# Performance work log

Hardware: AMD Instinct MI355X
Metric: run time of the kernel (lower is better)

## Reference

```python
import jax, jax.numpy as jnp
import numpy as np

N_NODES = 100000
N_EDGES = 1600000
D_IN = 128
D_OUT = 128
NEG_SLOPE = 0.01  # torch F.leaky_relu default


def setup_inputs() -> dict:
    key = jax.random.key(0)
    k1, k2, k3, k4, k5 = jax.random.split(key, 5)
    h = jax.random.normal(k1, (N_NODES, D_IN), dtype=jnp.float32)
    # nn.Linear default init scale ~ 1/sqrt(fan_in)
    W = jax.random.normal(k2, (D_IN, D_OUT), dtype=jnp.float32) / np.sqrt(D_IN)
    attn_w = jax.random.normal(k3, (2 * D_OUT,), dtype=jnp.float32) / np.sqrt(2 * D_OUT)
    edge_src = jax.random.randint(k4, (N_EDGES,), 0, N_NODES, dtype=jnp.int32)
    edge_dst = jax.random.randint(k5, (N_EDGES,), 0, N_NODES, dtype=jnp.int32)
    return {"h": h, "W": W, "attn_w": attn_w, "edge_src": edge_src, "edge_dst": edge_dst}


def reference(h, W, attn_w, edge_src, edge_dst):
    n = h.shape[0]
    d = W.shape[1]
    z = h @ W                                   # [N, d]
    # attention_func(cat([z_src, z_dst])) == z_src @ a[:d] + z_dst @ a[d:]
    s_src = z @ attn_w[:d]                      # [N]
    s_dst = z @ attn_w[d:]                      # [N]
    e = jax.nn.leaky_relu(s_src[edge_src] + s_dst[edge_dst], NEG_SLOPE)  # [E]
    # segment softmax over incoming edges of each dst node
    m = jax.ops.segment_max(e, edge_dst, num_segments=n)   # [N], -inf for empty
    ex = jnp.exp(e - m[edge_dst])                           # [E]
    denom = jax.ops.segment_sum(ex, edge_dst, num_segments=n)  # [N]
    alpha = ex / denom[edge_dst]                             # [E]
    # weighted neighbor sum: sum_j alpha_ij * z_j
    out = jax.ops.segment_sum(alpha[:, None] * z[edge_src], edge_dst, num_segments=n)
    return out
```

## Files before the change

### kernel.cpp

```cpp
#include <hip/hip_runtime.h>

#define D 128
#define NEG_SLOPE 0.01f
#define BSHIFT 7
#define B1 1024
#define SCHUNK 4096
#define SLOT 2560

typedef __attribute__((ext_vector_type(8))) short short8;
typedef __attribute__((ext_vector_type(4))) float floatx4;

__device__ __forceinline__ unsigned f2bf_rne(float x) {
    unsigned u = __float_as_uint(x);
    return (u + 0x7fffu + ((u >> 16) & 1u)) >> 16;
}
#define BF_LO(u) __uint_as_float((u) << 16)
#define BF_HI(u) __uint_as_float((u) & 0xffff0000u)

__global__ __launch_bounds__(256) void prep_wfrag(const float* __restrict__ W,
                                                  unsigned short* __restrict__ whi,
                                                  unsigned short* __restrict__ wlo,
                                                  int* __restrict__ gcur) {
    if (blockIdx.x == 0) {
        for (int i = threadIdx.x; i < B1; i += 256) gcur[i] = i * SLOT;
    }
    const int idx = blockIdx.x * 256 + threadIdx.x;
    const int j    = idx & 7;
    const int lane = (idx >> 3) & 63;
    const int tk   = idx >> 9;
    const int kk = tk & 3, ct = tk >> 2;
    const int k = kk * 32 + (lane >> 4) * 8 + j;
    const int n = ct * 16 + (lane & 15);
    const float x = W[k * D + n];
    const unsigned hi = f2bf_rne(x);
    const float hf = __uint_as_float(hi << 16);
    whi[idx] = (unsigned short)hi;
    wlo[idx] = (unsigned short)(__float_as_uint(x - hf) >> 16);
}

__global__ __launch_bounds__(1024) void sort_scatter(const int* __restrict__ esrc,
                                                     const int* __restrict__ edst,
                                                     int* __restrict__ gcur,
                                                     int* __restrict__ pairs, int E) {
    __shared__ int cnt[B1], exc[B1], gbs[B1], cur[B1];
    __shared__ int spk[SCHUNK];
    __shared__ unsigned short sbkt[SCHUNK];
    __shared__ int wtot[16];
    const int t = threadIdx.x;
    const int lane = t & 63, wv = t >> 6;
    cnt[t] = 0; cur[t] = 0;
    __syncthreads();

    const int e0 = blockIdx.x * SCHUNK;
    const int n  = min(SCHUNK, E - e0);

    int pk[4], bk[4];
    const int i0 = t * 4;
    if (i0 + 3 < n) {
        const int4 dv = *(const int4*)&edst[e0 + i0];
        const int4 sv = *(const int4*)&esrc[e0 + i0];
        const int dd[4] = {dv.x, dv.y, dv.z, dv.w};
        const int ss[4] = {sv.x, sv.y, sv.z, sv.w};
#pragma unroll
        for (int k = 0; k < 4; ++k) {
            bk[k] = dd[k] >> BSHIFT;
            pk[k] = (ss[k] << BSHIFT) | (dd[k] & 127);
            atomicAdd(&cnt[bk[k]], 1);
        }
    } else {
#pragma unroll
        for (int k = 0; k < 4; ++k) {
            const int i = i0 + k;
            if (i < n) {
                const int d = edst[e0 + i];
                const int s = esrc[e0 + i];
                bk[k] = d >> BSHIFT;
                pk[k] = (s << BSHIFT) | (d & 127);
                atomicAdd(&cnt[bk[k]], 1);
            } else {
                bk[k] = -1;
            }
        }
    }
    __syncthreads();

    const int c = cnt[t];
    int incl = c;
#pragma unroll
    for (int o = 1; o < 64; o <<= 1) {
        int v = __shfl_up(incl, o, 64);
        if (lane >= o) incl += v;
    }
    if (lane == 63) wtot[wv] = incl;
    __syncthreads();
    int wpre = 0;
#pragma unroll
    for (int i = 0; i < 16; ++i) wpre += (i < wv) ? wtot[i] : 0;
    exc[t] = wpre + incl - c;
    if (c > 0) gbs[t] = atomicAdd(&gcur[t], c);
    __syncthreads();

#pragma unroll
    for (int k = 0; k < 4; ++k) {
        if (bk[k] >= 0) {
            const int p = exc[bk[k]] + atomicAdd(&cur[bk[k]], 1);
            spk[p]  = pk[k];
            sbkt[p] = (unsigned short)bk[k];
        }
    }
    __syncthreads();

    for (int i = t; i < n; i += 1024) {
        const int b = sbkt[i];
        const int pos = gbs[b] + (i - exc[b]);
        if (pos < (b + 1) * SLOT) pairs[pos] = spk[i];
    }
}

__global__ __launch_bounds__(256) void fine_build(const int* __restrict__ pairs,
                                                  const int* __restrict__ gcur,
                                                  int* __restrict__ beg,
                                                  int* __restrict__ ncnt,
                                                  int* __restrict__ adj, int N) {
    __shared__ int cnt[128], sc[128], cur[128];
    const int b = blockIdx.x;
    const int base = b << BSHIFT;
    const int nd = min(128, N - base);
    const int t = threadIdx.x;
    const int s0 = b * SLOT;
    const int e1 = min(gcur[b], s0 + SLOT);
    if (t < 128) { cnt[t] = 0; cur[t] = 0; }
    __syncthreads();
    for (int i = s0 + t; i < e1; i += 256)
        atomicAdd(&cnt[pairs[i] & 127], 1);
    __syncthreads();
    if (t < 128) sc[t] = cnt[t];
    __syncthreads();
    for (int off = 1; off < 128; off <<= 1) {
        int v = (t < 128 && t >= off) ? sc[t - off] : 0;
        __syncthreads();
        if (t < 128) sc[t] += v;
        __syncthreads();
    }
    if (t < nd) {
        beg[base + t]  = s0 + sc[t] - cnt[t];
        ncnt[base + t] = cnt[t];
    }
    __syncthreads();
    for (int i = s0 + t; i < e1; i += 256) {
        const int pkv = pairs[i];
        const int d = pkv & 127;
        const int pos = s0 + (sc[d] - cnt[d]) + atomicAdd(&cur[d], 1);
        adj[pos] = pkv >> BSHIFT;
    }
}

__global__ __launch_bounds__(256) void gemm_zs(const float* __restrict__ h,
                                               const unsigned short* __restrict__ whi,
                                               const unsigned short* __restrict__ wlo,
                                               const float* __restrict__ aw,
                                               unsigned short* __restrict__ z,
                                               float* __restrict__ s_src,
                                               float* __restrict__ s_dst, int N) {
    const int t = threadIdx.x;
    const int lane = t & 63, quad = lane >> 4, l16 = lane & 15;
    const int rowbase = blockIdx.x * 64 + (t >> 6) * 16;
    const int arow = min(rowbase + l16, N - 1);
    const float* __restrict__ hrow = h + (size_t)arow * D;

    floatx4 acc[8];
#pragma unroll
    for (int ct = 0; ct < 8; ++ct) acc[ct] = (floatx4){0.f, 0.f, 0.f, 0.f};

#pragma unroll
    for (int kk = 0; kk < 4; ++kk) {
        const int k0 = kk * 32 + quad * 8;
        float4 x0 = *(const float4*)&hrow[k0];
        float4 x1 = *(const float4*)&hrow[k0 + 4];
        float xs[8] = {x0.x, x0.y, x0.z, x0.w, x1.x, x1.y, x1.z, x1.w};
        union { short8 v; unsigned short u[8]; } ahi, alo;
#pragma unroll
        for (int i = 0; i < 8; ++i) {
            unsigned hi = f2bf_rne(xs[i]);
            float hf = __uint_as_float(hi << 16);
            ahi.u[i] = (unsigned short)hi;
            alo.u[i] = (unsigned short)(__float_as_uint(xs[i] - hf) >> 16);
        }
#pragma unroll
        for (int ct = 0; ct < 8; ++ct) {
            const int fo = ((ct * 4 + kk) * 64 + lane) * 8;
            short8 bhi = *(const short8*)&whi[fo];
            short8 blo = *(const short8*)&wlo[fo];
            acc[ct] = __builtin_amdgcn_mfma_f32_16x16x32_bf16(ahi.v, bhi, acc[ct], 0, 0, 0);
            acc[ct] = __builtin_amdgcn_mfma_f32_16x16x32_bf16(alo.v, bhi, acc[ct], 0, 0, 0);
            acc[ct] = __builtin_amdgcn_mfma_f32_16x16x32_bf16(ahi.v, blo, acc[ct], 0, 0, 0);
        }
    }

#pragma unroll
    for (int ct = 0; ct < 8; ++ct)
#pragma unroll
        for (int reg = 0; reg < 4; ++reg) {
            int r = rowbase + quad * 4 + reg;
            if (r < N)
                z[(size_t)r * D + ct * 16 + l16] = (unsigned short)f2bf_rne(acc[ct][reg]);
        }

    float ps[4] = {0.f, 0.f, 0.f, 0.f}, pd[4] = {0.f, 0.f, 0.f, 0.f};
#pragma unroll
    for (int ct = 0; ct < 8; ++ct) {
        float as = aw[ct * 16 + l16];
        float ad = aw[128 + ct * 16 + l16];
#pragma unroll
        for (int reg = 0; reg < 4; ++reg) {
            ps[reg] = fmaf(acc[ct][reg], as, ps[reg]);
            pd[reg] = fmaf(acc[ct][reg], ad, pd[reg]);
        }
    }
#pragma unroll
    for (int reg = 0; reg < 4; ++reg)
#pragma unroll
        for (int o = 1; o < 16; o <<= 1) {
            ps[reg] += __shfl_xor(ps[reg], o, 64);
            pd[reg] += __shfl_xor(pd[reg], o, 64);
        }
    if (l16 == 0) {
#pragma unroll
        for (int reg = 0; reg < 4; ++reg) {
            int r = rowbase + quad * 4 + reg;
            if (r < N) { s_src[r] = ps[reg]; s_dst[r] = pd[reg]; }
        }
    }
}

__global__ __launch_bounds__(256) void aggregate(const unsigned short* __restrict__ z,
                                                 const float* __restrict__ s_src,
                                                 const float* __restrict__ s_dst,
                                                 const int* __restrict__ beg_,
                                                 const int* __restrict__ ncnt_,
                                                 const int* __restrict__ adj,
                                                 float* __restrict__ out,
                                                 int nodeBase, int nEnd) {
    const int lane = threadIdx.x & 63;
    const int half = lane >> 5;
    const int l32  = lane & 31;
    const int q2   = l32 >> 4;
    const int l16  = lane & 15;
    const int hb   = half << 5;
    const int pairBase = nodeBase + blockIdx.x * 8 + (threadIdx.x >> 6) * 2;
    if (pairBase >= nEnd) return;
    const int nodeA = pairBase, nodeB = pairBase + 1;
    const int cA = ncnt_[nodeA], bA = beg_[nodeA];
    int cB = 0, bB = 0;
    if (nodeB < nEnd) { cB = ncnt_[nodeB]; bB = beg_[nodeB]; }

    auto fma8 = [&](float* ac, float w, const uint4& v) {
        ac[0] = fmaf(w, BF_LO(v.x), ac[0]); ac[1] = fmaf(w, BF_HI(v.x), ac[1]);
        ac[2] = fmaf(w, BF_LO(v.y), ac[2]); ac[3] = fmaf(w, BF_HI(v.y), ac[3]);
        ac[4] = fmaf(w, BF_LO(v.z), ac[4]); ac[5] = fmaf(w, BF_HI(v.z), ac[5]);
        ac[6] = fmaf(w, BF_LO(v.w), ac[6]); ac[7] = fmaf(w, BF_HI(v.w), ac[7]);
    };

    if (max(cA, cB) <= 32) {
        const int myn = pairBase + half;
        const int valid = myn < nEnd;
        const int mb  = half ? bB : bA;
        const int mc  = half ? cB : cA;
        const float sd = s_dst[valid ? myn : 0];
        int s = 0; float e = -INFINITY;
        if (l32 < mc) {
            s = adj[mb + l32];
            float tt = s_src[s] + sd;
            e = (tt >= 0.f) ? tt : NEG_SLOPE * tt;
        }
        int sj[4]; uint4 zv[4];
#pragma unroll
        for (int u = 0; u < 4; ++u) sj[u] = __shfl(s, hb + u * 2 + q2, 64);
#pragma unroll
        for (int u = 0; u < 4; ++u)
            zv[u] = *(const uint4*)&z[(size_t)sj[u] * D + l16 * 8];

        float mx = e;
#pragma unroll
        for (int o = 16; o; o >>= 1) mx = fmaxf(mx, __shfl_xor(mx, o, 64));
        float ex = (l32 < mc) ? __expf(e - mx) : 0.f;
        float sum = ex;
#pragma unroll
        for (int o = 16; o; o >>= 1) sum += __shfl_xor(sum, o, 64);
        const float inv = (mc > 0) ? 1.f / sum : 0.f;
        const float w = ex * inv;

        float a[8] = {0.f,0.f,0.f,0.f,0.f,0.f,0.f,0.f};
        float bacc[8] = {0.f,0.f,0.f,0.f,0.f,0.f,0.f,0.f};
#pragma unroll
        for (int u = 0; u < 4; ++u) {
            const int ji = u * 2 + q2;
            float wj = __shfl(w, hb + ji, 64);
            wj = (ji < mc) ? wj : 0.f;
            fma8((u & 1) ? bacc : a, wj, zv[u]);
        }
        for (int jj = 8; jj < mc; jj += 8) {
            int ji2[4]; float wj[4]; int sj2[4];
#pragma unroll
            for (int u = 0; u < 4; ++u) {
                ji2[u] = jj + u * 2 + q2;
                wj[u]  = __shfl(w, hb + ji2[u], 64);
                sj2[u] = __shfl(s, hb + ji2[u], 64);
                wj[u]  = (ji2[u] < mc) ? wj[u] : 0.f;
            }
            uint4 z0 = *(const uint4*)&z[(size_t)sj2[0] * D + l16 * 8];
            uint4 z1 = *(const uint4*)&z[(size_t)sj2[1] * D + l16 * 8];
            uint4 z2 = *(const uint4*)&z[(size_t)sj2[2] * D + l16 * 8];
            uint4 z3 = *(const uint4*)&z[(size_t)sj2[3] * D + l16 * 8];
            fma8(a, wj[0], z0);
            fma8(bacc, wj[1], z1);
            fma8(a, wj[2], z2);
            fma8(bacc, wj[3], z3);
        }
#pragma unroll
        for (int i = 0; i < 8; ++i) {
            a[i] += bacc[i];
            a[i] += __shfl_xor(a[i], 16, 64);
        }
        if (q2 == 0 && valid) {
            float* o = &out[(size_t)myn * D + l16 * 8];
            *(float4*)o       = make_float4(a[0], a[1], a[2], a[3]);
            *(float4*)(o + 4) = make_float4(a[4], a[5], a[6], a[7]);
        }
        return;
    }

    const int q = lane >> 4;
    for (int which = 0; which < 2; ++which) {
        const int myn = which ? nodeB : nodeA;
        if (myn >= nEnd) break;
        const int mb = which ? bB : bA;
        const int mc = which ? cB : cA;
        const float sd = s_dst[myn];
        float a[8] = {0.f,0.f,0.f,0.f,0.f,0.f,0.f,0.f};
        float bacc[8] = {0.f,0.f,0.f,0.f,0.f,0.f,0.f,0.f};
        float mx = -INFINITY;
        for (int j = lane; j < mc; j += 64) {
            float tt = s_src[adj[mb + j]] + sd;
            tt = (tt >= 0.f) ? tt : NEG_SLOPE * tt;
            mx = fmaxf(mx, tt);
        }
#pragma unroll
        for (int o = 32; o; o >>= 1) mx = fmaxf(mx, __shfl_xor(mx, o, 64));
        float sum = 0.f;
        for (int j = lane; j < mc; j += 64) {
            float tt = s_src[adj[mb + j]] + sd;
            tt = (tt >= 0.f) ? tt : NEG_SLOPE * tt;
            sum += __expf(tt - mx);
        }
#pragma unroll
        for (int o = 32; o; o >>= 1) sum += __shfl_xor(sum, o, 64);
        const float inv = (mc > 0) ? 1.f / sum : 0.f;
        for (int base2 = 0; base2 < mc; base2 += 64) {
            const int cc = min(64, mc - base2);
            int s = 0; float w = 0.f;
            if (lane < cc) {
                s = adj[mb + base2 + lane];
                float tt = s_src[s] + sd;
                tt = (tt >= 0.f) ? tt : NEG_SLOPE * tt;
                w = __expf(tt - mx) * inv;
            }
            for (int jj = 0; jj < cc; jj += 8) {
                const int ja = jj + q;
                const int jb = ja + 4;
                float wa = __shfl(w, ja, 64); int sa = __shfl(s, ja, 64);
                float wb = __shfl(w, jb, 64); int sb = __shfl(s, jb, 64);
                wa = (ja < cc) ? wa : 0.f;
                wb = (jb < cc) ? wb : 0.f;
                uint4 za = *(const uint4*)&z[(size_t)sa * D + l16 * 8];
                uint4 zb = *(const uint4*)&z[(size_t)sb * D + l16 * 8];
                fma8(a, wa, za);
                fma8(bacc, wb, zb);
            }
        }
#pragma unroll
        for (int i = 0; i < 8; ++i) {
            a[i] += bacc[i];
            a[i] += __shfl_xor(a[i], 16, 64);
            a[i] += __shfl_xor(a[i], 32, 64);
        }
        if (q == 0) {
            float* o = &out[(size_t)myn * D + l16 * 8];
            *(float4*)o       = make_float4(a[0], a[1], a[2], a[3]);
            *(float4*)(o + 4) = make_float4(a[4], a[5], a[6], a[7]);
        }
    }
}

extern "C" void kernel_launch(void* const* d_in, const int* in_sizes, int n_in,
                              void* d_out, int out_size, void* d_ws, size_t ws_size,
                              hipStream_t stream) {
    const float* h    = (const float*)d_in[0];
    const float* W    = (const float*)d_in[1];
    const float* aw   = (const float*)d_in[2];
    const int*   esrc = (const int*)d_in[3];
    const int*   edst = (const int*)d_in[4];
    float* out = (float*)d_out;

    const int N = in_sizes[0] / D;
    const int E = in_sizes[3];
    const int NB1   = (N + 127) >> BSHIFT;
    const int NSORT = (E + SCHUNK - 1) / SCHUNK;

    char* p = (char*)d_ws;
    auto carve = [&](size_t bytes) {
        void* r = (void*)p;
        p += (bytes + 255) & ~size_t(255);
        return r;
    };
    unsigned short* z = (unsigned short*)carve(size_t(N) * D * sizeof(unsigned short));
    float* s_src  = (float*)carve(size_t(N) * sizeof(float));
    float* s_dst  = (float*)carve(size_t(N) * sizeof(float));
    int*   pairs  = (int*)carve(size_t(NB1) * SLOT * sizeof(int));
    int*   adj    = (int*)carve(size_t(NB1) * SLOT * sizeof(int));
    int*   beg    = (int*)carve(size_t(N) * sizeof(int));
    int*   ncnt   = (int*)carve(size_t(N) * sizeof(int));
    int*   gcur   = (int*)carve(size_t(B1) * sizeof(int));
    unsigned short* whi = (unsigned short*)carve(16384 * sizeof(unsigned short));
    unsigned short* wlo = (unsigned short*)carve(16384 * sizeof(unsigned short));
    (void)ws_size; (void)n_in; (void)out_size;

    prep_wfrag<<<64, 256, 0, stream>>>(W, whi, wlo, gcur);
    sort_scatter<<<NSORT, 1024, 0, stream>>>(esrc, edst, gcur, pairs, E);
    fine_build<<<NB1, 256, 0, stream>>>(pairs, gcur, beg, ncnt, adj, N);
    gemm_zs<<<(N + 63) / 64, 256, 0, stream>>>(h, whi, wlo, aw, z, s_src, s_dst, N);
    const int NH = (N / 2) & ~1;
    aggregate<<<(NH + 7) / 8, 256, 0, stream>>>(z, s_src, s_dst, beg, ncnt, adj, out, 0, NH);
    aggregate<<<(N - NH + 7) / 8, 256, 0, stream>>>(z, s_src, s_dst, beg, ncnt, adj, out, NH, N);
}
```

Baseline: 227.2 us.

## Privatize per-wave bucket counters, hoist GEMM loads, merge aggregate launches

After: 218.9 us. 1.04x faster.

```diff
diff --git a/kernel.cpp b/kernel.cpp
--- a/kernel.cpp
+++ b/kernel.cpp
@@ -122,19 +122,25 @@
                                                   int* __restrict__ beg,
                                                   int* __restrict__ ncnt,
                                                   int* __restrict__ adj, int N) {
-    __shared__ int cnt[128], sc[128], cur[128];
+    __shared__ int cnt[4][128], woff[4][128], cur[4][128];
+    __shared__ int sc[128];
     const int b = blockIdx.x;
     const int base = b << BSHIFT;
     const int nd = min(128, N - base);
     const int t = threadIdx.x;
+    const int wv = t >> 6;
     const int s0 = b * SLOT;
     const int e1 = min(gcur[b], s0 + SLOT);
-    if (t < 128) { cnt[t] = 0; cur[t] = 0; }
+    for (int i = t; i < 512; i += 256) { (&cnt[0][0])[i] = 0; (&cur[0][0])[i] = 0; }
     __syncthreads();
     for (int i = s0 + t; i < e1; i += 256)
-        atomicAdd(&cnt[pairs[i] & 127], 1);
-    __syncthreads();
-    if (t < 128) sc[t] = cnt[t];
+        atomicAdd(&cnt[wv][pairs[i] & 127], 1);
+    __syncthreads();
+    if (t < 128) {
+        const int c0 = cnt[0][t], c1 = cnt[1][t], c2 = cnt[2][t];
+        woff[0][t] = 0; woff[1][t] = c0; woff[2][t] = c0 + c1; woff[3][t] = c0 + c1 + c2;
+        sc[t] = c0 + c1 + c2 + cnt[3][t];
+    }
     __syncthreads();
     for (int off = 1; off < 128; off <<= 1) {
         int v = (t < 128 && t >= off) ? sc[t - off] : 0;
@@ -142,60 +148,70 @@
         if (t < 128) sc[t] += v;
         __syncthreads();
     }
-    if (t < nd) {
-        beg[base + t]  = s0 + sc[t] - cnt[t];
-        ncnt[base + t] = cnt[t];
+    if (t < 128) {
+        const int tot = cnt[0][t] + cnt[1][t] + cnt[2][t] + cnt[3][t];
+        const int excl = sc[t] - tot;
+        if (t < nd) { beg[base + t] = s0 + excl; ncnt[base + t] = tot; }
+        woff[0][t] += excl; woff[1][t] += excl; woff[2][t] += excl; woff[3][t] += excl;
     }
     __syncthreads();
     for (int i = s0 + t; i < e1; i += 256) {
         const int pkv = pairs[i];
         const int d = pkv & 127;
-        const int pos = s0 + (sc[d] - cnt[d]) + atomicAdd(&cur[d], 1);
+        const int pos = s0 + woff[wv][d] + atomicAdd(&cur[wv][d], 1);
         adj[pos] = pkv >> BSHIFT;
     }
 }
 
-__global__ __launch_bounds__(256) void gemm_zs(const float* __restrict__ h,
-                                               const unsigned short* __restrict__ whi,
-                                               const unsigned short* __restrict__ wlo,
-                                               const float* __restrict__ aw,
-                                               unsigned short* __restrict__ z,
-                                               float* __restrict__ s_src,
-                                               float* __restrict__ s_dst, int N) {
+__global__ __launch_bounds__(256, 3) void gemm_zs(const float* __restrict__ h,
+                                                  const unsigned short* __restrict__ whi,
+                                                  const unsigned short* __restrict__ wlo,
+                                                  const float* __restrict__ aw,
+                                                  unsigned short* __restrict__ z,
+                                                  float* __restrict__ s_src,
+                                                  float* __restrict__ s_dst, int N) {
     const int t = threadIdx.x;
     const int lane = t & 63, quad = lane >> 4, l16 = lane & 15;
     const int rowbase = blockIdx.x * 64 + (t >> 6) * 16;
     const int arow = min(rowbase + l16, N - 1);
     const float* __restrict__ hrow = h + (size_t)arow * D;
 
-    floatx4 acc[8];
-#pragma unroll
-    for (int ct = 0; ct < 8; ++ct) acc[ct] = (floatx4){0.f, 0.f, 0.f, 0.f};
-
+    float4 hx[8];
 #pragma unroll
     for (int kk = 0; kk < 4; ++kk) {
         const int k0 = kk * 32 + quad * 8;
-        float4 x0 = *(const float4*)&hrow[k0];
-        float4 x1 = *(const float4*)&hrow[k0 + 4];
-        float xs[8] = {x0.x, x0.y, x0.z, x0.w, x1.x, x1.y, x1.z, x1.w};
-        union { short8 v; unsigned short u[8]; } ahi, alo;
+        hx[kk * 2]     = *(const float4*)&hrow[k0];
+        hx[kk * 2 + 1] = *(const float4*)&hrow[k0 + 4];
+    }
+    union { short8 v; unsigned short u[8]; } ahi[4], alo[4];
+#pragma unroll
+    for (int kk = 0; kk < 4; ++kk) {
+        const float xs[8] = {hx[kk*2].x, hx[kk*2].y, hx[kk*2].z, hx[kk*2].w,
+                             hx[kk*2+1].x, hx[kk*2+1].y, hx[kk*2+1].z, hx[kk*2+1].w};
 #pragma unroll
         for (int i = 0; i < 8; ++i) {
-            unsigned hi = f2bf_rne(xs[i]);
-            float hf = __uint_as_float(hi << 16);
-            ahi.u[i] = (unsigned short)hi;
-            alo.u[i] = (unsigned short)(__float_as_uint(xs[i] - hf) >> 16);
-        }
+            const unsigned hi = f2bf_rne(xs[i]);
+            const float hf = __uint_as_float(hi << 16);
+            ahi[kk].u[i] = (unsigned short)hi;
+            alo[kk].u[i] = (unsigned short)(__float_as_uint(xs[i] - hf) >> 16);
+        }
+    }
+
+    floatx4 acc[8];
+#pragma unroll
+    for (int ct = 0; ct < 8; ++ct) acc[ct] = (floatx4){0.f, 0.f, 0.f, 0.f};
+
+#pragma unroll
+    for (int kk = 0; kk < 4; ++kk)
 #pragma unroll
         for (int ct = 0; ct < 8; ++ct) {
             const int fo = ((ct * 4 + kk) * 64 + lane) * 8;
             short8 bhi = *(const short8*)&whi[fo];
             short8 blo = *(const short8*)&wlo[fo];
-            acc[ct] = __builtin_amdgcn_mfma_f32_16x16x32_bf16(ahi.v, bhi, acc[ct], 0, 0, 0);
-            acc[ct] = __builtin_amdgcn_mfma_f32_16x16x32_bf16(alo.v, bhi, acc[ct], 0, 0, 0);
-            acc[ct] = __builtin_amdgcn_mfma_f32_16x16x32_bf16(ahi.v, blo, acc[ct], 0, 0, 0);
-        }
-    }
+            acc[ct] = __builtin_amdgcn_mfma_f32_16x16x32_bf16(ahi[kk].v, bhi, acc[ct], 0, 0, 0);
+            acc[ct] = __builtin_amdgcn_mfma_f32_16x16x32_bf16(alo[kk].v, bhi, acc[ct], 0, 0, 0);
+            acc[ct] = __builtin_amdgcn_mfma_f32_16x16x32_bf16(ahi[kk].v, blo, acc[ct], 0, 0, 0);
+        }
 
 #pragma unroll
     for (int ct = 0; ct < 8; ++ct)
@@ -239,20 +255,19 @@
                                                  const int* __restrict__ beg_,
                                                  const int* __restrict__ ncnt_,
                                                  const int* __restrict__ adj,
-                                                 float* __restrict__ out,
-                                                 int nodeBase, int nEnd) {
+                                                 float* __restrict__ out, int N) {
     const int lane = threadIdx.x & 63;
     const int half = lane >> 5;
     const int l32  = lane & 31;
     const int q2   = l32 >> 4;
     const int l16  = lane & 15;
     const int hb   = half << 5;
-    const int pairBase = nodeBase + blockIdx.x * 8 + (threadIdx.x >> 6) * 2;
-    if (pairBase >= nEnd) return;
+    const int pairBase = blockIdx.x * 8 + (threadIdx.x >> 6) * 2;
+    if (pairBase >= N) return;
     const int nodeA = pairBase, nodeB = pairBase + 1;
     const int cA = ncnt_[nodeA], bA = beg_[nodeA];
     int cB = 0, bB = 0;
-    if (nodeB < nEnd) { cB = ncnt_[nodeB]; bB = beg_[nodeB]; }
+    if (nodeB < N) { cB = ncnt_[nodeB]; bB = beg_[nodeB]; }
 
     auto fma8 = [&](float* ac, float w, const uint4& v) {
         ac[0] = fmaf(w, BF_LO(v.x), ac[0]); ac[1] = fmaf(w, BF_HI(v.x), ac[1]);
@@ -263,10 +278,9 @@
 
     if (max(cA, cB) <= 32) {
         const int myn = pairBase + half;
-        const int valid = myn < nEnd;
         const int mb  = half ? bB : bA;
         const int mc  = half ? cB : cA;
-        const float sd = s_dst[valid ? myn : 0];
+        const float sd = s_dst[myn < N ? myn : 0];
         int s = 0; float e = -INFINITY;
         if (l32 < mc) {
             s = adj[mb + l32];
@@ -322,7 +336,7 @@
             a[i] += bacc[i];
             a[i] += __shfl_xor(a[i], 16, 64);
         }
-        if (q2 == 0 && valid) {
+        if (q2 == 0 && myn < N) {
             float* o = &out[(size_t)myn * D + l16 * 8];
             *(float4*)o       = make_float4(a[0], a[1], a[2], a[3]);
             *(float4*)(o + 4) = make_float4(a[4], a[5], a[6], a[7]);
@@ -333,7 +347,7 @@
     const int q = lane >> 4;
     for (int which = 0; which < 2; ++which) {
         const int myn = which ? nodeB : nodeA;
-        if (myn >= nEnd) break;
+        if (myn >= N) break;
         const int mb = which ? bB : bA;
         const int mc = which ? cB : cA;
         const float sd = s_dst[myn];
@@ -429,7 +443,5 @@
     sort_scatter<<<NSORT, 1024, 0, stream>>>(esrc, edst, gcur, pairs, E);
     fine_build<<<NB1, 256, 0, stream>>>(pairs, gcur, beg, ncnt, adj, N);
     gemm_zs<<<(N + 63) / 64, 256, 0, stream>>>(h, whi, wlo, aw, z, s_src, s_dst, N);
-    const int NH = (N / 2) & ~1;
-    aggregate<<<(NH + 7) / 8, 256, 0, stream>>>(z, s_src, s_dst, beg, ncnt, adj, out, 0, NH);
-    aggregate<<<(N - NH + 7) / 8, 256, 0, stream>>>(z, s_src, s_dst, beg, ncnt, adj, out, NH, N);
-}
+    aggregate<<<(N + 7) / 8, 256, 0, stream>>>(z, s_src, s_dst, beg, ncnt, adj, out, N);
+}
```
